# Optimization experiments

Hardware: AMD Instinct MI355X
Metric: run time of the kernel (lower is better)

Reference implementation:

```python
import jax, jax.numpy as jnp
import numpy as np

BS, SEQ, ENC, DEC, HEADS, INTERM = 32, 2048, 512, 512, 8, 128
IH = INTERM * HEADS


def setup_inputs() -> dict:
    key = jax.random.key(0)
    ks = jax.random.split(key, 16)
    s = 0.02
    return {
        "enc": jax.random.normal(ks[0], (BS, SEQ, ENC), jnp.float32),
        "dec": jax.random.normal(ks[1], (BS, 1, DEC + ENC), jnp.float32),
        "kappa": jax.random.uniform(ks[2], (BS, 1, HEADS), jnp.float32),
        "mask": jnp.ones((BS, SEQ, 1), jnp.float32),
        "Wv": jax.random.normal(ks[3], (ENC, IH), jnp.float32) * s,
        "bv": jnp.zeros((IH,), jnp.float32),
        "Wq": jax.random.normal(ks[4], (DEC + ENC, IH), jnp.float32) * s,
        "bq": jnp.zeros((IH,), jnp.float32),
        "Wf": jax.random.normal(ks[5], (IH, HEADS), jnp.float32) * s,
        "bf": jnp.zeros((HEADS,), jnp.float32),
        "Wb": jax.random.normal(ks[6], (DEC + ENC, HEADS), jnp.float32) * s,
        "bb": jnp.zeros((HEADS,), jnp.float32),
        "Wk": jax.random.normal(ks[7], (DEC + ENC, HEADS), jnp.float32) * s,
        "bk": jnp.zeros((HEADS,), jnp.float32),
        "Wfc": jax.random.normal(ks[8], (ENC * HEADS, ENC), jnp.float32) * s,
        "bfc": jnp.zeros((ENC,), jnp.float32),
    }


def reference(enc, dec, kappa, mask, Wv, bv, Wq, bq, Wf, bf, Wb, bb, Wk, bk, Wfc, bfc):
    bs, seq_len, _ = enc.shape
    sp = jax.nn.softplus
    value = enc @ Wv + bv                      # (bs, seq, IH)
    query = dec @ Wq + bq                      # (bs, 1, IH), broadcasts over seq
    alpha = sp(jnp.tanh(query + value) @ Wf + bf) * mask   # (bs, seq, heads)
    beta = sp(dec @ Wb + bb)                   # (bs, 1, heads)
    kappa = kappa + sp(dec @ Wk + bk)          # (bs, 1, heads)
    u = jnp.arange(seq_len, dtype=enc.dtype)[None, :, None]
    score = alpha * jnp.exp(-beta * (kappa - u) ** 2)       # (bs, seq, heads)
    # weighted reduction over seq: (bs, heads, enc) then flatten in heads-major order
    context = jnp.einsum("bsh,bse->bhe", score, enc).reshape(bs, -1)
    context = context @ Wfc + bfc              # (bs, enc)
    return context[:, None, :], kappa, score
```

## Files before the change

### kernel.cpp

```cpp
#include <hip/hip_runtime.h>
#include <cstdint>
#include <cstddef>

#define BSZ    32
#define SEQL   2048
#define ENCD   512
#define DE     1024
#define NHEADS 8
#define IHD    1024

typedef unsigned short u16;
typedef __bf16 bf16x8 __attribute__((ext_vector_type(8)));
typedef float floatx4 __attribute__((ext_vector_type(4)));
typedef unsigned short u16x8 __attribute__((ext_vector_type(8)));

__device__ __forceinline__ u16 f2bf(float f) {
    unsigned int u = __float_as_uint(f);
    u = (u + 0x7FFFu + ((u >> 16) & 1u)) >> 16;
    return (u16)u;
}
__device__ __forceinline__ float bf2f(u16 v) {
    return __uint_as_float(((unsigned int)v) << 16);
}
__device__ __forceinline__ float softplus_f(float x) {
    return fmaxf(x, 0.0f) + log1pf(__expf(-fabsf(x)));
}
__device__ __forceinline__ float tanh_fast(float x) {
    const float e = __expf(2.0f * x);
    return 1.0f - 2.0f / (e + 1.0f);
}
__device__ __forceinline__ void async_cp16(u16* lds, const u16* g) {
    __builtin_amdgcn_global_load_lds(
        (const __attribute__((address_space(1))) unsigned int*)g,
        (__attribute__((address_space(3))) unsigned int*)lds, 16, 0, 0);
}

__global__ __launch_bounds__(256) void conv_enc_kernel(const float* __restrict__ in,
                                                       u16* __restrict__ out) {
    const size_t i = (size_t)blockIdx.x * 256 + threadIdx.x;
    const float4* p = (const float4*)in + i * 2;
    const float4 a = p[0], b = p[1];
    u16x8 o;
    o[0] = f2bf(a.x); o[1] = f2bf(a.y); o[2] = f2bf(a.z); o[3] = f2bf(a.w);
    o[4] = f2bf(b.x); o[5] = f2bf(b.y); o[6] = f2bf(b.z); o[7] = f2bf(b.w);
    *((u16x8*)out + i) = o;
}

__global__ __launch_bounds__(256) void conv_w_kernel(const float* __restrict__ Wv,
                                                     const float* __restrict__ Wf,
                                                     u16* __restrict__ WvT,
                                                     u16* __restrict__ wfb) {
    __shared__ float tile[64 * 65];
    const int bid = blockIdx.x, tid = threadIdx.x;
    if (bid == 128) {
        for (int i = tid; i < 8192; i += 256) {
            const int j   = i & 7;
            const int fr8 = (i >> 3) & 7;
            const int qd  = (i >> 6) & 3;
            const int ks  = (i >> 8) & 3;
            const int nn  = i >> 10;
            const int row = nn * 128 + ks * 32 + qd * 8 + j;
            wfb[i] = f2bf(Wf[row * NHEADS + fr8]);
        }
        return;
    }
    const int nt = bid & 15, kt = bid >> 4;
    for (int i = tid; i < 4096; i += 256) {
        const int kk = i >> 6, nn = i & 63;
        tile[kk * 65 + nn] = Wv[(size_t)(kt * 64 + kk) * IHD + nt * 64 + nn];
    }
    __syncthreads();
    for (int i = tid; i < 4096; i += 256) {
        const int nn = i >> 6, kk = i & 63;
        WvT[(size_t)(nt * 64 + nn) * 512 + kt * 64 + kk] = f2bf(tile[kk * 65 + nn]);
    }
}

__global__ __launch_bounds__(256) void prep_kernel(
    const float* __restrict__ dec, const float* __restrict__ kappa_in,
    const float* __restrict__ Wq, const float* __restrict__ bq,
    const float* __restrict__ bv,
    const float* __restrict__ Wb, const float* __restrict__ bb,
    const float* __restrict__ Wk, const float* __restrict__ bk,
    float* __restrict__ query_ws, float* __restrict__ beta_ws,
    float* __restrict__ kappa_out)
{
    __shared__ float s_dec[DE];
    __shared__ float s_red[256];
    const int b = blockIdx.x, y = blockIdx.y, tid = threadIdx.x;
    for (int i = tid; i < DE; i += 256) s_dec[i] = dec[b * DE + i];
    __syncthreads();

    if (y < 32) {
        const int cl = tid & 31, kg = tid >> 5;
        const int col = y * 32 + cl;
        float a = 0.f;
        const float* w = Wq + col;
        #pragma unroll 4
        for (int k = kg * 128; k < kg * 128 + 128; ++k)
            a = fmaf(s_dec[k], w[(size_t)k * IHD], a);
        s_red[tid] = a;
        __syncthreads();
        if (tid < 32) {
            float s = 0.f;
            #pragma unroll
            for (int i = 0; i < 8; ++i) s += s_red[i * 32 + tid];
            query_ws[(size_t)b * IHD + col] = s + bq[col] + bv[col];
        }
    } else {
        const int h = tid & 7, kg = tid >> 3;
        float ab = 0.f, ak = 0.f;
        for (int k = kg * 32; k < kg * 32 + 32; ++k) {
            const float d = s_dec[k];
            ab = fmaf(d, Wb[k * NHEADS + h], ab);
            ak = fmaf(d, Wk[k * NHEADS + h], ak);
        }
        s_red[tid] = ab;
        __syncthreads();
        for (int off = 128; off >= 8; off >>= 1) {
            if (tid < off) s_red[tid] += s_red[tid + off];
            __syncthreads();
        }
        const float abT = (tid < 8) ? s_red[tid] : 0.f;
        __syncthreads();
        s_red[tid] = ak;
        __syncthreads();
        for (int off = 128; off >= 8; off >>= 1) {
            if (tid < off) s_red[tid] += s_red[tid + off];
            __syncthreads();
        }
        if (tid < 8) {
            beta_ws[b * NHEADS + tid]   = softplus_f(bb[tid] + abT);
            kappa_out[b * NHEADS + tid] = kappa_in[b * NHEADS + tid]
                                        + softplus_f(bk[tid] + s_red[tid]);
        }
    }
}

#define BM 128
#define BN 128
#define BK 64

__global__ __launch_bounds__(256, 2) void gemm_score_kernel(
    const u16* __restrict__ encb, const u16* __restrict__ wvT,
    const u16* __restrict__ wfb2, const float* __restrict__ bf_g,
    const float* __restrict__ mask, const float* __restrict__ query_ws,
    const float* __restrict__ beta_ws, const float* __restrict__ kappa_out,
    float* __restrict__ score_out)
{
    __shared__ __align__(16) unsigned char smem[65536];

    const int tid  = threadIdx.x;
    const int m0   = blockIdx.x * BM;
    const int b    = blockIdx.x >> 4;
    const int lane = tid & 63;
    const int w    = tid >> 6;
    const int wr   = w >> 1, wc = w & 1;
    const int fr   = lane & 15, quad = lane >> 4;

    int mA[4], csA[4];
    #pragma unroll
    for (int r = 0; r < 4; ++r) {
        const int s = r * 256 + tid;
        mA[r]  = s >> 3;
        csA[r] = (s & 7) ^ (mA[r] & 7);
    }

    auto stage = [&](int bufsel, int it) {
        u16* Ab = (u16*)(smem + bufsel * 32768);
        u16* Bb = Ab + 8192;
        const int nn2 = it >> 3, kt2 = it & 7;
        const size_t aoff = (size_t)kt2 * 64;
        const size_t boff = (size_t)nn2 * (128 * 512) + (size_t)kt2 * 64;
        #pragma unroll
        for (int r = 0; r < 4; ++r) {
            async_cp16(Ab + (r * 256 + (tid & 192)) * 8,
                       encb + (size_t)(m0 + mA[r]) * 512 + aoff + csA[r] * 8);
            async_cp16(Bb + (r * 256 + (tid & 192)) * 8,
                       wvT + (size_t)mA[r] * 512 + boff + csA[r] * 8);
        }
    };

    floatx4 acc2[2] = {};

    stage(0, 0);

    for (int nn = 0; nn < 8; ++nn) {
        const int n0 = nn * 128;
        float qv[4];
        bf16x8 wfr[4];
        floatx4 acc[4][4] = {};

        #pragma unroll
        for (int kt = 0; kt < 8; ++kt) {
            const int it = nn * 8 + kt;
            if (kt < 7) {
                stage((it + 1) & 1, it + 1);
            } else if (nn < 7) {
                stage((it + 1) & 1, it + 1);
            }
            if (kt == 0) {
                #pragma unroll
                for (int nt = 0; nt < 4; ++nt)
                    qv[nt] = query_ws[(size_t)b * IHD + n0 + wc * 64 + nt * 16 + fr];
                #pragma unroll
                for (int ks = 0; ks < 4; ++ks)
                    wfr[ks] = *(const bf16x8*)&wfb2[((nn * 4 + ks) * 4 + quad) * 64
                                                    + (fr & 7) * 8];
            }
            if (kt == 7 && nn == 7) {
                asm volatile("s_waitcnt vmcnt(0)" ::: "memory");
            } else if (kt == 0) {
                asm volatile("s_waitcnt vmcnt(16)" ::: "memory");
            } else {
                asm volatile("s_waitcnt vmcnt(8)" ::: "memory");
            }
            __builtin_amdgcn_sched_barrier(0);
            __builtin_amdgcn_s_barrier();

            u16* Ab = (u16*)(smem + (it & 1) * 32768);
            u16* Bb = Ab + 8192;
            __builtin_amdgcn_s_setprio(1);
            #pragma unroll
            for (int s2 = 0; s2 < 2; ++s2) {
                bf16x8 af[4], bfr[4];
                #pragma unroll
                for (int mt = 0; mt < 4; ++mt) {
                    const int ma = wr * 64 + mt * 16 + fr;
                    const int ca = (s2 * 4 + quad) ^ (ma & 7);
                    af[mt] = *(const bf16x8*)&Ab[ma * 64 + ca * 8];
                }
                #pragma unroll
                for (int nt = 0; nt < 4; ++nt) {
                    const int nb = wc * 64 + nt * 16 + fr;
                    const int cb = (s2 * 4 + quad) ^ (nb & 7);
                    bfr[nt] = *(const bf16x8*)&Bb[nb * 64 + cb * 8];
                }
                #pragma unroll
                for (int mt = 0; mt < 4; ++mt)
                    #pragma unroll
                    for (int nt = 0; nt < 4; ++nt)
                        acc[mt][nt] = __builtin_amdgcn_mfma_f32_16x16x32_bf16(
                            af[mt], bfr[nt], acc[mt][nt], 0, 0, 0);
            }
            __builtin_amdgcn_s_setprio(0);
            __builtin_amdgcn_sched_barrier(0);
            __builtin_amdgcn_s_barrier();
        }

        u16* tT = (u16*)(smem + 32768);
        #pragma unroll
        for (int mt = 0; mt < 4; ++mt) {
            #pragma unroll
            for (int nt = 0; nt < 4; ++nt) {
                const int col = wc * 64 + nt * 16 + fr;
                #pragma unroll
                for (int reg = 0; reg < 4; ++reg) {
                    const int row = wr * 64 + mt * 16 + quad * 4 + reg;
                    ((__bf16*)tT)[row * 128 + (col ^ ((row & 7) << 3))] =
                        (__bf16)tanh_fast(acc[mt][nt][reg] + qv[nt]);
                }
            }
        }
        asm volatile("s_waitcnt lgkmcnt(0)" ::: "memory");
        __builtin_amdgcn_sched_barrier(0);
        __builtin_amdgcn_s_barrier();

        #pragma unroll
        for (int t = 0; t < 2; ++t) {
            const int row = w * 32 + t * 16 + fr;
            #pragma unroll
            for (int ks = 0; ks < 4; ++ks) {
                const bf16x8 ta = *(const bf16x8*)
                    &tT[row * 128 + ((ks * 32 + quad * 8) ^ ((row & 7) << 3))];
                acc2[t] = __builtin_amdgcn_mfma_f32_16x16x32_bf16(ta, wfr[ks], acc2[t], 0, 0, 0);
            }
        }
        __builtin_amdgcn_sched_barrier(0);
        __builtin_amdgcn_s_barrier();
    }

    if (fr < NHEADS) {
        const float bfh = bf_g[fr];
        const float bet = beta_ws[b * NHEADS + fr];
        const float kap = kappa_out[b * NHEADS + fr];
        #pragma unroll
        for (int t = 0; t < 2; ++t) {
            #pragma unroll
            for (int reg = 0; reg < 4; ++reg) {
                const int row = m0 + w * 32 + t * 16 + quad * 4 + reg;
                const int s = row & 2047;
                const float alpha = softplus_f(acc2[t][reg] + bfh) * mask[row];
                const float du = kap - (float)s;
                score_out[(size_t)row * NHEADS + fr] = alpha * __expf(-bet * du * du);
            }
        }
    }
}

__global__ __launch_bounds__(256) void context_kernel(
    const u16* __restrict__ encb, const float* __restrict__ score,
    float* __restrict__ ctx_part)
{
    __shared__ float s_sc[128 * NHEADS];
    const int b = blockIdx.x, sc = blockIdx.y, tid = threadIdx.x;
    const int lane = tid & 63, w = tid >> 6;
    const int e8 = lane * 8;
    const size_t srow0 = (size_t)b * SEQL + sc * 128;

    for (int i = tid; i < 128 * NHEADS; i += 256)
        s_sc[i] = score[srow0 * NHEADS + i];
    __syncthreads();

    float acc0[8] = {}, acc1[8] = {};
    const u16* ep = encb + srow0 * ENCD + e8;
    #pragma unroll 4
    for (int s = 0; s < 128; ++s) {
        const u16x8 ev = *(const u16x8*)(ep + (size_t)s * ENCD);
        const float2 sc2 = *(const float2*)&s_sc[s * NHEADS + 2 * w];
        #pragma unroll
        for (int j = 0; j < 8; ++j) {
            const float e = bf2f(ev[j]);
            acc0[j] = fmaf(sc2.x, e, acc0[j]);
            acc1[j] = fmaf(sc2.y, e, acc1[j]);
        }
    }

    float* outp = ctx_part + ((size_t)sc * BSZ + b) * (NHEADS * ENCD);
    *(float4*)&outp[(2 * w + 0) * ENCD + e8]     = make_float4(acc0[0], acc0[1], acc0[2], acc0[3]);
    *(float4*)&outp[(2 * w + 0) * ENCD + e8 + 4] = make_float4(acc0[4], acc0[5], acc0[6], acc0[7]);
    *(float4*)&outp[(2 * w + 1) * ENCD + e8]     = make_float4(acc1[0], acc1[1], acc1[2], acc1[3]);
    *(float4*)&outp[(2 * w + 1) * ENCD + e8 + 4] = make_float4(acc1[4], acc1[5], acc1[6], acc1[7]);
}

__global__ __launch_bounds__(256) void ctx_reduce_kernel(
    const float* __restrict__ part, float* __restrict__ ctx_ws)
{
    const int i = blockIdx.x * 256 + threadIdx.x;
    float a = 0.f;
    #pragma unroll
    for (int sc = 0; sc < 16; ++sc)
        a += part[(size_t)sc * 131072 + i];
    ctx_ws[i] = a;
}

__global__ __launch_bounds__(256) void final_kernel(
    const float* __restrict__ ctx_ws, const float* __restrict__ Wfc,
    const float* __restrict__ bfc, float* __restrict__ out_ctx)
{
    __shared__ float s_ctx[32][128];
    const int jc = blockIdx.x, ks = blockIdx.y, tid = threadIdx.x;
    const int jl = tid & 31, bg = tid >> 5;
    const int j = jc * 32 + jl;
    float a0 = 0.f, a1 = 0.f, a2 = 0.f, a3 = 0.f;

    for (int t = 0; t < 4; ++t) {
        const int k0 = ks * 512 + t * 128;
        __syncthreads();
        for (int i = tid; i < 32 * 128; i += 256) {
            const int bb2 = i >> 7, kk = i & 127;
            s_ctx[bb2][kk] = ctx_ws[(size_t)bb2 * (NHEADS * ENCD) + k0 + kk];
        }
        __syncthreads();
        for (int kk = 0; kk < 128; ++kk) {
            const float wv = Wfc[(size_t)(k0 + kk) * ENCD + j];
            a0 = fmaf(s_ctx[bg * 4 + 0][kk], wv, a0);
            a1 = fmaf(s_ctx[bg * 4 + 1][kk], wv, a1);
            a2 = fmaf(s_ctx[bg * 4 + 2][kk], wv, a2);
            a3 = fmaf(s_ctx[bg * 4 + 3][kk], wv, a3);
        }
    }
    const float bias = (ks == 0) ? bfc[j] : 0.0f;
    atomicAdd(&out_ctx[(bg * 4 + 0) * ENCD + j], a0 + bias);
    atomicAdd(&out_ctx[(bg * 4 + 1) * ENCD + j], a1 + bias);
    atomicAdd(&out_ctx[(bg * 4 + 2) * ENCD + j], a2 + bias);
    atomicAdd(&out_ctx[(bg * 4 + 3) * ENCD + j], a3 + bias);
}

extern "C" void kernel_launch(void* const* d_in, const int* in_sizes, int n_in,
                              void* d_out, int out_size, void* d_ws, size_t ws_size,
                              hipStream_t stream)
{
    const float* enc   = (const float*)d_in[0];
    const float* dec   = (const float*)d_in[1];
    const float* kapin = (const float*)d_in[2];
    const float* mask  = (const float*)d_in[3];
    const float* Wv    = (const float*)d_in[4];
    const float* bv    = (const float*)d_in[5];
    const float* Wq    = (const float*)d_in[6];
    const float* bq    = (const float*)d_in[7];
    const float* Wf    = (const float*)d_in[8];
    const float* bf    = (const float*)d_in[9];
    const float* Wb    = (const float*)d_in[10];
    const float* bb    = (const float*)d_in[11];
    const float* Wk    = (const float*)d_in[12];
    const float* bk    = (const float*)d_in[13];
    const float* Wfc   = (const float*)d_in[14];
    const float* bfc   = (const float*)d_in[15];

    float* out       = (float*)d_out;
    float* out_ctx   = out;
    float* out_kappa = out + 16384;
    float* out_score = out + 16640;

    char* w = (char*)d_ws;
    u16*   enc_bf   = (u16*)w;
    float* ctx_part = (float*)(w + 67108864);
    u16*   wvT      = (u16*)(w + 75497472);
    float* q_ws     = (float*)(w + 76546048);
    float* beta_ws  = (float*)(w + 76677120);
    float* ctx_ws   = (float*)(w + 76678144);
    u16*   wfb      = (u16*)(w + 77202432);

    hipMemsetAsync(out_ctx, 0, 16384 * sizeof(float), stream);

    conv_enc_kernel<<<dim3(16384), dim3(256), 0, stream>>>(enc, enc_bf);
    conv_w_kernel<<<dim3(129), dim3(256), 0, stream>>>(Wv, Wf, wvT, wfb);

    prep_kernel<<<dim3(BSZ, 33), dim3(256), 0, stream>>>(
        dec, kapin, Wq, bq, bv, Wb, bb, Wk, bk, q_ws, beta_ws, out_kappa);

    gemm_score_kernel<<<dim3((BSZ * SEQL) / BM), dim3(256), 0, stream>>>(
        enc_bf, wvT, wfb, bf, mask, q_ws, beta_ws, out_kappa, out_score);

    context_kernel<<<dim3(BSZ, 16), dim3(256), 0, stream>>>(
        enc_bf, out_score, ctx_part);

    ctx_reduce_kernel<<<dim3(512), dim3(256), 0, stream>>>(ctx_part, ctx_ws);

    final_kernel<<<dim3(16, 8), dim3(256), 0, stream>>>(
        ctx_ws, Wfc, bfc, out_ctx);
}
```

Measured before the change: 437.1 us.

## Fuse prep kernels, load A fragments directly from global, fuse context into GEMM

Merges the enc conversion, weight transpose and query/beta/kappa prep into one launch. Inside the GEMM, the enc (A) operand is now loaded straight from global memory into registers with double-buffered fragments, and only the B tile is staged in LDS. The per-tile context reduction is fused into the GEMM epilogue using scores kept in LDS, which removes the separate context kernel and its reread of the scores. This cuts launch overhead and traffic, at the cost of more VGPR pressure and uncoalesced A loads that may hurt the GEMM main loop.

```diff
diff --git a/kernel.cpp b/kernel.cpp
--- a/kernel.cpp
+++ b/kernel.cpp
@@ -35,24 +35,46 @@
         (__attribute__((address_space(3))) unsigned int*)lds, 16, 0, 0);
 }
 
-__global__ __launch_bounds__(256) void conv_enc_kernel(const float* __restrict__ in,
-                                                       u16* __restrict__ out) {
-    const size_t i = (size_t)blockIdx.x * 256 + threadIdx.x;
-    const float4* p = (const float4*)in + i * 2;
-    const float4 a = p[0], b = p[1];
-    u16x8 o;
-    o[0] = f2bf(a.x); o[1] = f2bf(a.y); o[2] = f2bf(a.z); o[3] = f2bf(a.w);
-    o[4] = f2bf(b.x); o[5] = f2bf(b.y); o[6] = f2bf(b.z); o[7] = f2bf(b.w);
-    *((u16x8*)out + i) = o;
-}
-
-__global__ __launch_bounds__(256) void conv_w_kernel(const float* __restrict__ Wv,
-                                                     const float* __restrict__ Wf,
-                                                     u16* __restrict__ WvT,
-                                                     u16* __restrict__ wfb) {
-    __shared__ float tile[64 * 65];
+__global__ __launch_bounds__(256) void pre_kernel(
+    const float* __restrict__ enc, u16* __restrict__ enc_bf,
+    const float* __restrict__ Wv, const float* __restrict__ Wf,
+    u16* __restrict__ WvT, u16* __restrict__ wfb,
+    const float* __restrict__ dec, const float* __restrict__ kappa_in,
+    const float* __restrict__ Wq, const float* __restrict__ bq,
+    const float* __restrict__ bv,
+    const float* __restrict__ Wb, const float* __restrict__ bb,
+    const float* __restrict__ Wk, const float* __restrict__ bk,
+    float* __restrict__ query_ws, float* __restrict__ beta_ws,
+    float* __restrict__ kappa_out)
+{
+    __shared__ float sh[64 * 65];
     const int bid = blockIdx.x, tid = threadIdx.x;
-    if (bid == 128) {
+
+    if (bid < 16384) {
+        const size_t i = (size_t)bid * 256 + tid;
+        const float4* p = (const float4*)enc + i * 2;
+        const float4 a = p[0], b2 = p[1];
+        u16x8 o;
+        o[0] = f2bf(a.x);  o[1] = f2bf(a.y);  o[2] = f2bf(a.z);  o[3] = f2bf(a.w);
+        o[4] = f2bf(b2.x); o[5] = f2bf(b2.y); o[6] = f2bf(b2.z); o[7] = f2bf(b2.w);
+        *((u16x8*)enc_bf + i) = o;
+        return;
+    }
+    if (bid < 16512) {
+        const int tb = bid - 16384;
+        const int nt = tb & 15, kt = tb >> 4;
+        for (int i = tid; i < 4096; i += 256) {
+            const int kk = i >> 6, nn = i & 63;
+            sh[kk * 65 + nn] = Wv[(size_t)(kt * 64 + kk) * IHD + nt * 64 + nn];
+        }
+        __syncthreads();
+        for (int i = tid; i < 4096; i += 256) {
+            const int nn = i >> 6, kk = i & 63;
+            WvT[(size_t)(nt * 64 + nn) * 512 + kt * 64 + kk] = f2bf(sh[kk * 65 + nn]);
+        }
+        return;
+    }
+    if (bid == 16512) {
         for (int i = tid; i < 8192; i += 256) {
             const int j   = i & 7;
             const int fr8 = (i >> 3) & 7;
@@ -64,30 +86,10 @@
         }
         return;
     }
-    const int nt = bid & 15, kt = bid >> 4;
-    for (int i = tid; i < 4096; i += 256) {
-        const int kk = i >> 6, nn = i & 63;
-        tile[kk * 65 + nn] = Wv[(size_t)(kt * 64 + kk) * IHD + nt * 64 + nn];
-    }
-    __syncthreads();
-    for (int i = tid; i < 4096; i += 256) {
-        const int nn = i >> 6, kk = i & 63;
-        WvT[(size_t)(nt * 64 + nn) * 512 + kt * 64 + kk] = f2bf(tile[kk * 65 + nn]);
-    }
-}
-
-__global__ __launch_bounds__(256) void prep_kernel(
-    const float* __restrict__ dec, const float* __restrict__ kappa_in,
-    const float* __restrict__ Wq, const float* __restrict__ bq,
-    const float* __restrict__ bv,
-    const float* __restrict__ Wb, const float* __restrict__ bb,
-    const float* __restrict__ Wk, const float* __restrict__ bk,
-    float* __restrict__ query_ws, float* __restrict__ beta_ws,
-    float* __restrict__ kappa_out)
-{
-    __shared__ float s_dec[DE];
-    __shared__ float s_red[256];
-    const int b = blockIdx.x, y = blockIdx.y, tid = threadIdx.x;
+    const int p = bid - 16513;
+    const int b = p & 31, y = p >> 5;
+    float* s_dec = sh;
+    float* s_red = sh + DE;
     for (int i = tid; i < DE; i += 256) s_dec[i] = dec[b * DE + i];
     __syncthreads();
 
@@ -138,21 +140,22 @@
 }
 
 #define BM 128
-#define BN 128
-#define BK 64
-
-__global__ __launch_bounds__(256, 2) void gemm_score_kernel(
+
+__global__ __launch_bounds__(256, 2) void gemm_score_ctx_kernel(
     const u16* __restrict__ encb, const u16* __restrict__ wvT,
     const u16* __restrict__ wfb2, const float* __restrict__ bf_g,
     const float* __restrict__ mask, const float* __restrict__ query_ws,
     const float* __restrict__ beta_ws, const float* __restrict__ kappa_out,
-    float* __restrict__ score_out)
+    float* __restrict__ score_out, float* __restrict__ ctx_part)
 {
-    __shared__ __align__(16) unsigned char smem[65536];
+    __shared__ __align__(16) unsigned char smem[69632];
+    u16*   tT      = (u16*)(smem + 32768);
+    float* s_score = (float*)(smem + 65536);
 
     const int tid  = threadIdx.x;
     const int m0   = blockIdx.x * BM;
     const int b    = blockIdx.x >> 4;
+    const int sc   = blockIdx.x & 15;
     const int lane = tid & 63;
     const int w    = tid >> 6;
     const int wr   = w >> 1, wc = w & 1;
@@ -166,24 +169,83 @@
         csA[r] = (s & 7) ^ (mA[r] & 7);
     }
 
-    auto stage = [&](int bufsel, int it) {
-        u16* Ab = (u16*)(smem + bufsel * 32768);
-        u16* Bb = Ab + 8192;
-        const int nn2 = it >> 3, kt2 = it & 7;
-        const size_t aoff = (size_t)kt2 * 64;
-        const size_t boff = (size_t)nn2 * (128 * 512) + (size_t)kt2 * 64;
+    auto stageB = [&](int bufsel, int nn2, int kt2) {
+        u16* Bb = (u16*)(smem + bufsel * 16384);
+        const u16* src = wvT + (size_t)nn2 * 65536 + kt2 * 64;
         #pragma unroll
-        for (int r = 0; r < 4; ++r) {
-            async_cp16(Ab + (r * 256 + (tid & 192)) * 8,
-                       encb + (size_t)(m0 + mA[r]) * 512 + aoff + csA[r] * 8);
+        for (int r = 0; r < 4; ++r)
             async_cp16(Bb + (r * 256 + (tid & 192)) * 8,
-                       wvT + (size_t)mA[r] * 512 + boff + csA[r] * 8);
-        }
+                       src + (size_t)mA[r] * 512 + csA[r] * 8);
     };
 
+#define LOADA(DST, KT2)                                                        \
+    _Pragma("unroll")                                                          \
+    for (int mt_ = 0; mt_ < 4; ++mt_) {                                        \
+        _Pragma("unroll")                                                      \
+        for (int s2_ = 0; s2_ < 2; ++s2_)                                      \
+            DST[mt_][s2_] = *(const bf16x8*)&encb[                             \
+                (size_t)(m0 + wr * 64 + mt_ * 16 + fr) * 512                   \
+                + (KT2) * 64 + s2_ * 32 + quad * 8];                           \
+    }
+
+#define KT_STEP(KT, AUSE, ALOAD)                                               \
+    {                                                                          \
+        const int cur_ = (KT) & 1;                                             \
+        if ((KT) < 7 || nn < 7) {                                              \
+            const int nn2_ = ((KT) < 7) ? nn : nn + 1;                         \
+            const int kt2_ = ((KT) < 7) ? (KT) + 1 : 0;                        \
+            stageB(cur_ ^ 1, nn2_, kt2_);                                      \
+            LOADA(ALOAD, kt2_);                                                \
+        }                                                                      \
+        if ((KT) == 0) {                                                       \
+            _Pragma("unroll")                                                  \
+            for (int nt_ = 0; nt_ < 4; ++nt_)                                  \
+                qv[nt_] = query_ws[(size_t)b * IHD + n0 + wc * 64              \
+                                   + nt_ * 16 + fr];                           \
+            _Pragma("unroll")                                                  \
+            for (int ks_ = 0; ks_ < 4; ++ks_)                                  \
+                wfr[ks_] = *(const bf16x8*)&wfb2[((nn * 4 + ks_) * 4 + quad)   \
+                                                  * 64 + (fr & 7) * 8];        \
+        }                                                                      \
+        if ((KT) == 7) {                                                       \
+            if (nn == 7) { asm volatile("s_waitcnt vmcnt(0)" ::: "memory"); }  \
+            else         { asm volatile("s_waitcnt vmcnt(12)" ::: "memory"); } \
+        } else if ((KT) == 0) {                                                \
+            asm volatile("s_waitcnt vmcnt(20)" ::: "memory");                  \
+        } else {                                                               \
+            asm volatile("s_waitcnt vmcnt(12)" ::: "memory");                  \
+        }                                                                      \
+        __builtin_amdgcn_sched_barrier(0);                                     \
+        __builtin_amdgcn_s_barrier();       \
+        const u16* Bb = (const u16*)(smem + cur_ * 16384);                     \
+        __builtin_amdgcn_s_setprio(1);                                         \
+        _Pragma("unroll")                                                      \
+        for (int s2_ = 0; s2_ < 2; ++s2_) {                                    \
+            bf16x8 bfr[4];                                                     \
+            _Pragma("unroll")                                                  \
+            for (int nt_ = 0; nt_ < 4; ++nt_) {                                \
+                const int nb_ = wc * 64 + nt_ * 16 + fr;                       \
+                const int cb_ = (s2_ * 4 + quad) ^ (nb_ & 7);                  \
+                bfr[nt_] = *(const bf16x8*)&Bb[nb_ * 64 + cb_ * 8];            \
+            }                                                                  \
+            _Pragma("unroll")                                                  \
+            for (int mt_ = 0; mt_ < 4; ++mt_) {                                \
+                _Pragma("unroll")                                              \
+                for (int nt_ = 0; nt_ < 4; ++nt_)                              \
+                    acc[mt_][nt_] = __builtin_amdgcn_mfma_f32_16x16x32_bf16(   \
+                        AUSE[mt_][s2_], bfr[nt_], acc[mt_][nt_], 0, 0, 0);     \
+            }                                                                  \
+        }                                                                      \
+        __builtin_amdgcn_s_setprio(0);                                         \
+        __builtin_amdgcn_sched_barrier(0);                                     \
+        __builtin_amdgcn_s_barrier();       \
+    }
+
     floatx4 acc2[2] = {};
-
-    stage(0, 0);
+    bf16x8 afp0[4][2], afp1[4][2];
+
+    stageB(0, 0, 0);
+    LOADA(afp0, 0);
 
     for (int nn = 0; nn < 8; ++nn) {
         const int n0 = nn * 128;
@@ -191,64 +253,15 @@
         bf16x8 wfr[4];
         floatx4 acc[4][4] = {};
 
-        #pragma unroll
-        for (int kt = 0; kt < 8; ++kt) {
-            const int it = nn * 8 + kt;
-            if (kt < 7) {
-                stage((it + 1) & 1, it + 1);
-            } else if (nn < 7) {
-                stage((it + 1) & 1, it + 1);
-            }
-            if (kt == 0) {
-                #pragma unroll
-                for (int nt = 0; nt < 4; ++nt)
-                    qv[nt] = query_ws[(size_t)b * IHD + n0 + wc * 64 + nt * 16 + fr];
-                #pragma unroll
-                for (int ks = 0; ks < 4; ++ks)
-                    wfr[ks] = *(const bf16x8*)&wfb2[((nn * 4 + ks) * 4 + quad) * 64
-                                                    + (fr & 7) * 8];
-            }
-            if (kt == 7 && nn == 7) {
-                asm volatile("s_waitcnt vmcnt(0)" ::: "memory");
-            } else if (kt == 0) {
-                asm volatile("s_waitcnt vmcnt(16)" ::: "memory");
-            } else {
-                asm volatile("s_waitcnt vmcnt(8)" ::: "memory");
-            }
-            __builtin_amdgcn_sched_barrier(0);
-            __builtin_amdgcn_s_barrier();
-
-            u16* Ab = (u16*)(smem + (it & 1) * 32768);
-            u16* Bb = Ab + 8192;
-            __builtin_amdgcn_s_setprio(1);
-            #pragma unroll
-            for (int s2 = 0; s2 < 2; ++s2) {
-                bf16x8 af[4], bfr[4];
-                #pragma unroll
-                for (int mt = 0; mt < 4; ++mt) {
-                    const int ma = wr * 64 + mt * 16 + fr;
-                    const int ca = (s2 * 4 + quad) ^ (ma & 7);
-                    af[mt] = *(const bf16x8*)&Ab[ma * 64 + ca * 8];
-                }
-                #pragma unroll
-                for (int nt = 0; nt < 4; ++nt) {
-                    const int nb = wc * 64 + nt * 16 + fr;
-                    const int cb = (s2 * 4 + quad) ^ (nb & 7);
-                    bfr[nt] = *(const bf16x8*)&Bb[nb * 64 + cb * 8];
-                }
-                #pragma unroll
-                for (int mt = 0; mt < 4; ++mt)
-                    #pragma unroll
-                    for (int nt = 0; nt < 4; ++nt)
-                        acc[mt][nt] = __builtin_amdgcn_mfma_f32_16x16x32_bf16(
-                            af[mt], bfr[nt], acc[mt][nt], 0, 0, 0);
-            }
-            __builtin_amdgcn_s_setprio(0);
-            __builtin_amdgcn_sched_barrier(0);
-            __builtin_amdgcn_s_barrier();
-        }
-
-        u16* tT = (u16*)(smem + 32768);
+        KT_STEP(0, afp0, afp1)
+        KT_STEP(1, afp1, afp0)
+        KT_STEP(2, afp0, afp1)
+        KT_STEP(3, afp1, afp0)
+        KT_STEP(4, afp0, afp1)
+        KT_STEP(5, afp1, afp0)
+        KT_STEP(6, afp0, afp1)
+        KT_STEP(7, afp1, afp0)
+
         #pragma unroll
         for (int mt = 0; mt < 4; ++mt) {
             #pragma unroll
@@ -276,8 +289,6 @@
                 acc2[t] = __builtin_amdgcn_mfma_f32_16x16x32_bf16(ta, wfr[ks], acc2[t], 0, 0, 0);
             }
         }
-        __builtin_amdgcn_sched_barrier(0);
-        __builtin_amdgcn_s_barrier();
     }
 
     if (fr < NHEADS) {
@@ -288,49 +299,41 @@
         for (int t = 0; t < 2; ++t) {
             #pragma unroll
             for (int reg = 0; reg < 4; ++reg) {
-                const int row = m0 + w * 32 + t * 16 + quad * 4 + reg;
-                const int s = row & 2047;
-                const float alpha = softplus_f(acc2[t][reg] + bfh) * mask[row];
+                const int row  = w * 32 + t * 16 + quad * 4 + reg;
+                const int grow = m0 + row;
+                const int s = grow & 2047;
+                const float alpha = softplus_f(acc2[t][reg] + bfh) * mask[grow];
                 const float du = kap - (float)s;
-                score_out[(size_t)row * NHEADS + fr] = alpha * __expf(-bet * du * du);
+                const float v = alpha * __expf(-bet * du * du);
+                score_out[(size_t)grow * NHEADS + fr] = v;
+                s_score[row * NHEADS + fr] = v;
             }
         }
     }
-}
-
-__global__ __launch_bounds__(256) void context_kernel(
-    const u16* __restrict__ encb, const float* __restrict__ score,
-    float* __restrict__ ctx_part)
-{
-    __shared__ float s_sc[128 * NHEADS];
-    const int b = blockIdx.x, sc = blockIdx.y, tid = threadIdx.x;
-    const int lane = tid & 63, w = tid >> 6;
-    const int e8 = lane * 8;
-    const size_t srow0 = (size_t)b * SEQL + sc * 128;
-
-    for (int i = tid; i < 128 * NHEADS; i += 256)
-        s_sc[i] = score[srow0 * NHEADS + i];
-    __syncthreads();
-
-    float acc0[8] = {}, acc1[8] = {};
-    const u16* ep = encb + srow0 * ENCD + e8;
-    #pragma unroll 4
-    for (int s = 0; s < 128; ++s) {
-        const u16x8 ev = *(const u16x8*)(ep + (size_t)s * ENCD);
-        const float2 sc2 = *(const float2*)&s_sc[s * NHEADS + 2 * w];
-        #pragma unroll
-        for (int j = 0; j < 8; ++j) {
-            const float e = bf2f(ev[j]);
-            acc0[j] = fmaf(sc2.x, e, acc0[j]);
-            acc1[j] = fmaf(sc2.y, e, acc1[j]);
-        }
-    }
-
-    float* outp = ctx_part + ((size_t)sc * BSZ + b) * (NHEADS * ENCD);
-    *(float4*)&outp[(2 * w + 0) * ENCD + e8]     = make_float4(acc0[0], acc0[1], acc0[2], acc0[3]);
-    *(float4*)&outp[(2 * w + 0) * ENCD + e8 + 4] = make_float4(acc0[4], acc0[5], acc0[6], acc0[7]);
-    *(float4*)&outp[(2 * w + 1) * ENCD + e8]     = make_float4(acc1[0], acc1[1], acc1[2], acc1[3]);
-    *(float4*)&outp[(2 * w + 1) * ENCD + e8 + 4] = make_float4(acc1[4], acc1[5], acc1[6], acc1[7]);
+    asm volatile("s_waitcnt lgkmcnt(0)" ::: "memory");
+    __builtin_amdgcn_s_barrier();
+
+    {
+        float acc0[8] = {}, acc1[8] = {};
+        const u16* ep = encb + (size_t)m0 * 512 + lane * 8;
+        #pragma unroll 4
+        for (int s = 0; s < 128; ++s) {
+            const u16x8 ev = *(const u16x8*)(ep + (size_t)s * 512);
+            const float2 sc2 = *(const float2*)&s_score[s * NHEADS + 2 * w];
+            #pragma unroll
+            for (int j = 0; j < 8; ++j) {
+                const float e = bf2f(ev[j]);
+                acc0[j] = fmaf(sc2.x, e, acc0[j]);
+                acc1[j] = fmaf(sc2.y, e, acc1[j]);
+            }
+        }
+        const int e8 = lane * 8;
+        float* outp = ctx_part + ((size_t)sc * BSZ + b) * (NHEADS * ENCD);
+        *(float4*)&outp[(2 * w + 0) * ENCD + e8]     = make_float4(acc0[0], acc0[1], acc0[2], acc0[3]);
+        *(float4*)&outp[(2 * w + 0) * ENCD + e8 + 4] = make_float4(acc0[4], acc0[5], acc0[6], acc0[7]);
+        *(float4*)&outp[(2 * w + 1) * ENCD + e8]     = make_float4(acc1[0], acc1[1], acc1[2], acc1[3]);
+        *(float4*)&outp[(2 * w + 1) * ENCD + e8 + 4] = make_float4(acc1[4], acc1[5], acc1[6], acc1[7]);
+    }
 }
 
 __global__ __launch_bounds__(256) void ctx_reduce_kernel(
@@ -414,17 +417,13 @@
 
     hipMemsetAsync(out_ctx, 0, 16384 * sizeof(float), stream);
 
-    conv_enc_kernel<<<dim3(16384), dim3(256), 0, stream>>>(enc, enc_bf);
-    conv_w_kernel<<<dim3(129), dim3(256), 0, stream>>>(Wv, Wf, wvT, wfb);
-
-    prep_kernel<<<dim3(BSZ, 33), dim3(256), 0, stream>>>(
+    pre_kernel<<<dim3(16384 + 128 + 1 + 1056), dim3(256), 0, stream>>>(
+        enc, enc_bf, Wv, Wf, wvT, wfb,
         dec, kapin, Wq, bq, bv, Wb, bb, Wk, bk, q_ws, beta_ws, out_kappa);
 
-    gemm_score_kernel<<<dim3((BSZ * SEQL) / BM), dim3(256), 0, stream>>>(
-        enc_bf, wvT, wfb, bf, mask, q_ws, beta_ws, out_kappa, out_score);
-
-    context_kernel<<<dim3(BSZ, 16), dim3(256), 0, stream>>>(
-        enc_bf, out_score, ctx_part);
+    gemm_score_ctx_kernel<<<dim3((BSZ * SEQL) / BM), dim3(256), 0, stream>>>(
+        enc_bf, wvT, wfb, bf, mask, q_ws, beta_ws, out_kappa,
+        out_score, ctx_part);
 
     ctx_reduce_kernel<<<dim3(512), dim3(256), 0, stream>>>(ctx_part, ctx_ws);
 
```

After: 590.0 us. 35.0% more time.

## Fuse context reduction into score GEMM and merge prep kernels

Applied to the files above, without the earlier changes.

Merges the three preprocessing kernels (enc conversion, weight transpose/convert, query/beta/kappa prep) into one launch dispatched by block index. Folds the context weighted-sum into the GEMM+score kernel, so each block reuses its own score tile from shared memory and reads the enc rows it just used instead of launching a separate context kernel. This removes launch overhead and a global round-trip of the scores. In exchange, shared memory per block grows slightly, which may affect the two-blocks-per-CU occupancy, and the fused kernel carries a longer serial tail.

```diff
diff --git a/kernel.cpp b/kernel.cpp
--- a/kernel.cpp
+++ b/kernel.cpp
@@ -35,24 +35,46 @@
         (__attribute__((address_space(3))) unsigned int*)lds, 16, 0, 0);
 }
 
-__global__ __launch_bounds__(256) void conv_enc_kernel(const float* __restrict__ in,
-                                                       u16* __restrict__ out) {
-    const size_t i = (size_t)blockIdx.x * 256 + threadIdx.x;
-    const float4* p = (const float4*)in + i * 2;
-    const float4 a = p[0], b = p[1];
-    u16x8 o;
-    o[0] = f2bf(a.x); o[1] = f2bf(a.y); o[2] = f2bf(a.z); o[3] = f2bf(a.w);
-    o[4] = f2bf(b.x); o[5] = f2bf(b.y); o[6] = f2bf(b.z); o[7] = f2bf(b.w);
-    *((u16x8*)out + i) = o;
-}
-
-__global__ __launch_bounds__(256) void conv_w_kernel(const float* __restrict__ Wv,
-                                                     const float* __restrict__ Wf,
-                                                     u16* __restrict__ WvT,
-                                                     u16* __restrict__ wfb) {
-    __shared__ float tile[64 * 65];
+__global__ __launch_bounds__(256) void pre_kernel(
+    const float* __restrict__ enc, u16* __restrict__ enc_bf,
+    const float* __restrict__ Wv, const float* __restrict__ Wf,
+    u16* __restrict__ WvT, u16* __restrict__ wfb,
+    const float* __restrict__ dec, const float* __restrict__ kappa_in,
+    const float* __restrict__ Wq, const float* __restrict__ bq,
+    const float* __restrict__ bv,
+    const float* __restrict__ Wb, const float* __restrict__ bb,
+    const float* __restrict__ Wk, const float* __restrict__ bk,
+    float* __restrict__ query_ws, float* __restrict__ beta_ws,
+    float* __restrict__ kappa_out)
+{
+    __shared__ float sh[64 * 65];
     const int bid = blockIdx.x, tid = threadIdx.x;
-    if (bid == 128) {
+
+    if (bid < 16384) {
+        const size_t i = (size_t)bid * 256 + tid;
+        const float4* p = (const float4*)enc + i * 2;
+        const float4 a = p[0], b2 = p[1];
+        u16x8 o;
+        o[0] = f2bf(a.x);  o[1] = f2bf(a.y);  o[2] = f2bf(a.z);  o[3] = f2bf(a.w);
+        o[4] = f2bf(b2.x); o[5] = f2bf(b2.y); o[6] = f2bf(b2.z); o[7] = f2bf(b2.w);
+        *((u16x8*)enc_bf + i) = o;
+        return;
+    }
+    if (bid < 16512) {
+        const int tb = bid - 16384;
+        const int nt = tb & 15, kt = tb >> 4;
+        for (int i = tid; i < 4096; i += 256) {
+            const int kk = i >> 6, nn = i & 63;
+            sh[kk * 65 + nn] = Wv[(size_t)(kt * 64 + kk) * IHD + nt * 64 + nn];
+        }
+        __syncthreads();
+        for (int i = tid; i < 4096; i += 256) {
+            const int nn = i >> 6, kk = i & 63;
+            WvT[(size_t)(nt * 64 + nn) * 512 + kt * 64 + kk] = f2bf(sh[kk * 65 + nn]);
+        }
+        return;
+    }
+    if (bid == 16512) {
         for (int i = tid; i < 8192; i += 256) {
             const int j   = i & 7;
             const int fr8 = (i >> 3) & 7;
@@ -64,30 +86,10 @@
         }
         return;
     }
-    const int nt = bid & 15, kt = bid >> 4;
-    for (int i = tid; i < 4096; i += 256) {
-        const int kk = i >> 6, nn = i & 63;
-        tile[kk * 65 + nn] = Wv[(size_t)(kt * 64 + kk) * IHD + nt * 64 + nn];
-    }
-    __syncthreads();
-    for (int i = tid; i < 4096; i += 256) {
-        const int nn = i >> 6, kk = i & 63;
-        WvT[(size_t)(nt * 64 + nn) * 512 + kt * 64 + kk] = f2bf(tile[kk * 65 + nn]);
-    }
-}
-
-__global__ __launch_bounds__(256) void prep_kernel(
-    const float* __restrict__ dec, const float* __restrict__ kappa_in,
-    const float* __restrict__ Wq, const float* __restrict__ bq,
-    const float* __restrict__ bv,
-    const float* __restrict__ Wb, const float* __restrict__ bb,
-    const float* __restrict__ Wk, const float* __restrict__ bk,
-    float* __restrict__ query_ws, float* __restrict__ beta_ws,
-    float* __restrict__ kappa_out)
-{
-    __shared__ float s_dec[DE];
-    __shared__ float s_red[256];
-    const int b = blockIdx.x, y = blockIdx.y, tid = threadIdx.x;
+    const int p = bid - 16513;
+    const int b = p & 31, y = p >> 5;
+    float* s_dec = sh;
+    float* s_red = sh + DE;
     for (int i = tid; i < DE; i += 256) s_dec[i] = dec[b * DE + i];
     __syncthreads();
 
@@ -138,21 +140,22 @@
 }
 
 #define BM 128
-#define BN 128
-#define BK 64
-
-__global__ __launch_bounds__(256, 2) void gemm_score_kernel(
+
+__global__ __launch_bounds__(256, 2) void gemm_score_ctx_kernel(
     const u16* __restrict__ encb, const u16* __restrict__ wvT,
     const u16* __restrict__ wfb2, const float* __restrict__ bf_g,
     const float* __restrict__ mask, const float* __restrict__ query_ws,
     const float* __restrict__ beta_ws, const float* __restrict__ kappa_out,
-    float* __restrict__ score_out)
+    float* __restrict__ score_out, float* __restrict__ ctx_part)
 {
-    __shared__ __align__(16) unsigned char smem[65536];
+    __shared__ __align__(16) unsigned char smem[69632];
+    u16*   tT      = (u16*)(smem + 32768);
+    float* s_score = (float*)(smem + 65536);
 
     const int tid  = threadIdx.x;
     const int m0   = blockIdx.x * BM;
     const int b    = blockIdx.x >> 4;
+    const int sc   = blockIdx.x & 15;
     const int lane = tid & 63;
     const int w    = tid >> 6;
     const int wr   = w >> 1, wc = w & 1;
@@ -161,9 +164,9 @@
     int mA[4], csA[4];
     #pragma unroll
     for (int r = 0; r < 4; ++r) {
-        const int s = r * 256 + tid;
-        mA[r]  = s >> 3;
-        csA[r] = (s & 7) ^ (mA[r] & 7);
+        const int c = r * 256 + tid;
+        mA[r]  = c >> 3;
+        csA[r] = (c & 7) ^ (mA[r] & 7);
     }
 
     auto stage = [&](int bufsel, int it) {
@@ -176,7 +179,7 @@
         for (int r = 0; r < 4; ++r) {
             async_cp16(Ab + (r * 256 + (tid & 192)) * 8,
                        encb + (size_t)(m0 + mA[r]) * 512 + aoff + csA[r] * 8);
-            async_cp16(Bb + (r * 256 + (tid & 192)) * 8,
+            async_cp16(Bb + (size_t)(r * 256 + (tid & 192)) * 8,
                        wvT + (size_t)mA[r] * 512 + boff + csA[r] * 8);
         }
     };
@@ -194,11 +197,8 @@
         #pragma unroll
         for (int kt = 0; kt < 8; ++kt) {
             const int it = nn * 8 + kt;
-            if (kt < 7) {
+            if (kt < 7 || nn < 7)
                 stage((it + 1) & 1, it + 1);
-            } else if (nn < 7) {
-                stage((it + 1) & 1, it + 1);
-            }
             if (kt == 0) {
                 #pragma unroll
                 for (int nt = 0; nt < 4; ++nt)
@@ -248,7 +248,6 @@
             __builtin_amdgcn_s_barrier();
         }
 
-        u16* tT = (u16*)(smem + 32768);
         #pragma unroll
         for (int mt = 0; mt < 4; ++mt) {
             #pragma unroll
@@ -288,49 +287,41 @@
         for (int t = 0; t < 2; ++t) {
             #pragma unroll
             for (int reg = 0; reg < 4; ++reg) {
-                const int row = m0 + w * 32 + t * 16 + quad * 4 + reg;
-                const int s = row & 2047;
-                const float alpha = softplus_f(acc2[t][reg] + bfh) * mask[row];
+                const int row  = w * 32 + t * 16 + quad * 4 + reg;
+                const int grow = m0 + row;
+                const int s = grow & 2047;
+                const float alpha = softplus_f(acc2[t][reg] + bfh) * mask[grow];
                 const float du = kap - (float)s;
-                score_out[(size_t)row * NHEADS + fr] = alpha * __expf(-bet * du * du);
-            }
-        }
-    }
-}
-
-__global__ __launch_bounds__(256) void context_kernel(
-    const u16* __restrict__ encb, const float* __restrict__ score,
-    float* __restrict__ ctx_part)
-{
-    __shared__ float s_sc[128 * NHEADS];
-    const int b = blockIdx.x, sc = blockIdx.y, tid = threadIdx.x;
-    const int lane = tid & 63, w = tid >> 6;
-    const int e8 = lane * 8;
-    const size_t srow0 = (size_t)b * SEQL + sc * 128;
-
-    for (int i = tid; i < 128 * NHEADS; i += 256)
-        s_sc[i] = score[srow0 * NHEADS + i];
-    __syncthreads();
-
-    float acc0[8] = {}, acc1[8] = {};
-    const u16* ep = encb + srow0 * ENCD + e8;
-    #pragma unroll 4
-    for (int s = 0; s < 128; ++s) {
-        const u16x8 ev = *(const u16x8*)(ep + (size_t)s * ENCD);
-        const float2 sc2 = *(const float2*)&s_sc[s * NHEADS + 2 * w];
-        #pragma unroll
-        for (int j = 0; j < 8; ++j) {
-            const float e = bf2f(ev[j]);
-            acc0[j] = fmaf(sc2.x, e, acc0[j]);
-            acc1[j] = fmaf(sc2.y, e, acc1[j]);
-        }
-    }
-
-    float* outp = ctx_part + ((size_t)sc * BSZ + b) * (NHEADS * ENCD);
-    *(float4*)&outp[(2 * w + 0) * ENCD + e8]     = make_float4(acc0[0], acc0[1], acc0[2], acc0[3]);
-    *(float4*)&outp[(2 * w + 0) * ENCD + e8 + 4] = make_float4(acc0[4], acc0[5], acc0[6], acc0[7]);
-    *(float4*)&outp[(2 * w + 1) * ENCD + e8]     = make_float4(acc1[0], acc1[1], acc1[2], acc1[3]);
-    *(float4*)&outp[(2 * w + 1) * ENCD + e8 + 4] = make_float4(acc1[4], acc1[5], acc1[6], acc1[7]);
+                const float v = alpha * __expf(-bet * du * du);
+                score_out[(size_t)grow * NHEADS + fr] = v;
+                s_score[row * NHEADS + fr] = v;
+            }
+        }
+    }
+    asm volatile("s_waitcnt lgkmcnt(0)" ::: "memory");
+    __builtin_amdgcn_s_barrier();
+
+    {
+        float acc0[8] = {}, acc1[8] = {};
+        const u16* ep = encb + (size_t)m0 * 512 + lane * 8;
+        #pragma unroll 4
+        for (int s = 0; s < 128; ++s) {
+            const u16x8 ev = *(const u16x8*)(ep + (size_t)s * 512);
+            const float2 sc2 = *(const float2*)&s_score[s * NHEADS + 2 * w];
+            #pragma unroll
+            for (int j = 0; j < 8; ++j) {
+                const float e = bf2f(ev[j]);
+                acc0[j] = fmaf(sc2.x, e, acc0[j]);
+                acc1[j] = fmaf(sc2.y, e, acc1[j]);
+            }
+        }
+        const int e8 = lane * 8;
+        float* outp = ctx_part + ((size_t)sc * BSZ + b) * (NHEADS * ENCD);
+        *(float4*)&outp[(2 * w + 0) * ENCD + e8]     = make_float4(acc0[0], acc0[1], acc0[2], acc0[3]);
+        *(float4*)&outp[(2 * w + 0) * ENCD + e8 + 4] = make_float4(acc0[4], acc0[5], acc0[6], acc0[7]);
+        *(float4*)&outp[(2 * w + 1) * ENCD + e8]     = make_float4(acc1[0], acc1[1], acc1[2], acc1[3]);
+        *(float4*)&outp[(2 * w + 1) * ENCD + e8 + 4] = make_float4(acc1[4], acc1[5], acc1[6], acc1[7]);
+    }
 }
 
 __global__ __launch_bounds__(256) void ctx_reduce_kernel(
@@ -414,17 +405,13 @@
 
     hipMemsetAsync(out_ctx, 0, 16384 * sizeof(float), stream);
 
-    conv_enc_kernel<<<dim3(16384), dim3(256), 0, stream>>>(enc, enc_bf);
-    conv_w_kernel<<<dim3(129), dim3(256), 0, stream>>>(Wv, Wf, wvT, wfb);
-
-    prep_kernel<<<dim3(BSZ, 33), dim3(256), 0, stream>>>(
+    pre_kernel<<<dim3(16384 + 128 + 1 + 1056), dim3(256), 0, stream>>>(
+        enc, enc_bf, Wv, Wf, wvT, wfb,
         dec, kapin, Wq, bq, bv, Wb, bb, Wk, bk, q_ws, beta_ws, out_kappa);
 
-    gemm_score_kernel<<<dim3((BSZ * SEQL) / BM), dim3(256), 0, stream>>>(
-        enc_bf, wvT, wfb, bf, mask, q_ws, beta_ws, out_kappa, out_score);
-
-    context_kernel<<<dim3(BSZ, 16), dim3(256), 0, stream>>>(
-        enc_bf, out_score, ctx_part);
+    gemm_score_ctx_kernel<<<dim3((BSZ * SEQL) / BM), dim3(256), 0, stream>>>(
+        enc_bf, wvT, wfb, bf, mask, q_ws, beta_ws, out_kappa,
+        out_score, ctx_part);
 
     ctx_reduce_kernel<<<dim3(512), dim3(256), 0, stream>>>(ctx_part, ctx_ws);
 
```

Result: faster. 420.0 us (-3.9%).
